# Optimization experiments

Hardware: AMD Instinct MI355X
Metric: run time of the kernel (lower is better)

## Reference

```python
import jax, jax.numpy as jnp
import numpy as np

jax.config.update("jax_enable_x64", True)  # I-BERT's FixedPointMul runs in double precision

# I-BERT IntSoftmax constants
COEF0 = 0.35815147
COEF1 = 0.96963238 / COEF0
COEF2 = 1.0 / COEF0
X0 = -0.6931          # -ln(2)
N_EXP = 30            # large integer n in int_exp
MAX_BIT = 32
OUTPUT_BIT = 8
ACT_BIT = 16

B, H, S = 1, 12, 2048


def sg(x):
    return jax.lax.stop_gradient(x)


def ste_round(x):
    # straight-through round (matches torch round_ste / SymmetricQuantFunction backward)
    return x + sg(jnp.round(x) - x)


def ste_floor(x):
    return x + sg(jnp.floor(x) - x)


def sym_scale(x_min, x_max, bits):
    # symmetric_linear_quantization_params: scale = clamp(max(|min|,|max|),1e-8)/(2^(b-1)-1)
    n = 2 ** (bits - 1) - 1
    s = jnp.maximum(jnp.abs(x_min), jnp.abs(x_max))
    return sg(jnp.maximum(s, 1e-8) / n)


def fixedpoint_mul(pre_act, pre_sf, z_sf, bits):
    # I-BERT fixedpoint_mul: requantize pre_act (granularity pre_sf) to scale z_sf
    # using a 31-bit mantissa frexp decomposition, computed in float64.
    n = 2 ** (bits - 1) - 1
    z_int = ste_round(pre_act.astype(jnp.float64) / pre_sf.astype(jnp.float64))
    new_scale = sg((pre_sf / z_sf).astype(jnp.float64))
    e = jnp.floor(jnp.log2(jnp.abs(new_scale))) + 1.0   # frexp exponent
    m_int = jnp.round((new_scale / 2.0 ** e) * 2.0 ** 31)  # 31-bit mantissa
    out = ste_round(z_int * m_int / 2.0 ** (31.0 - e))
    return jnp.clip(out, -n - 1, n).astype(jnp.float32)


def quant_softmax(x):
    n16 = 2 ** (ACT_BIT - 1) - 1
    # ---- outer QuantAct(16, symmetric), specified min/max = data min/max ----
    sf = sym_scale(sg(x.min()), sg(x.max()), ACT_BIT)
    x_int = jnp.clip(ste_round(x / sf), -n16 - 1, n16)
    quant_x = x_int * sf  # dequantized activation returned by QuantAct
    # ---- IntSoftmax ----
    xi = quant_x / sf
    xi = xi - xi.max(axis=-1, keepdims=True)
    # int_exp: shift-based exponential, exp(x) = 2^(-q) * exp(r), r in (-ln2, 0]
    x0_int = sg(jnp.floor(X0 / sf))               # negative integer
    xi = jnp.maximum(xi, N_EXP * x0_int)
    q = ste_floor(xi / x0_int)
    r = xi - x0_int * q
    # int_polynomial: 2nd-order poly approximation of exp on (-ln2, 0]
    b_int = sg(jnp.floor(COEF1 / sf))
    c_int = sg(jnp.floor(COEF2 / sf ** 2))
    z = r * (r + b_int) + c_int
    exp_sf = sg(COEF0 * sf ** 2) / 2.0 ** N_EXP
    exp_int = jnp.maximum(ste_floor(z * 2.0 ** (N_EXP - q)), 0.0)
    # ---- inner QuantAct(16): requantize exp to 16 bits to avoid overflow ----
    act_sf = sym_scale(sg(exp_int.min()), sg(exp_int.max()), ACT_BIT)
    exp_int16 = fixedpoint_mul(exp_int, exp_sf, act_sf, ACT_BIT)
    # ---- integer normalization to output_bit fixed point ----
    s = exp_int16.sum(axis=-1, keepdims=True)
    factor = ste_floor(2.0 ** MAX_BIT / s)
    out_int = ste_floor(exp_int16 * factor / 2.0 ** (MAX_BIT - OUTPUT_BIT))
    out_sf = 1.0 / 2.0 ** OUTPUT_BIT
    return out_int * out_sf  # softmax probs quantized to 1/256 grid


def setup_inputs() -> dict:
    key = jax.random.key(0)
    x = jax.random.normal(key, (B, H, S, S), dtype=jnp.float32)
    return {"x": x}


def reference(x):
    return quant_softmax(x)
```

## Files before the change

kernel.cpp:

```cpp
#include <hip/hip_runtime.h>
#include <math.h>


#define ROW_S 2048
#define MM_BLOCKS 2048
#define MM_STRIDE (MM_BLOCKS * 256)

typedef float floatx4 __attribute__((ext_vector_type(4)));

struct Scalars {
    double exp_sf_d;
    double inv_exp_sf;
    double m_int;
    double inv_pow;
    float  sf;
    float  inv_sf;
    float  x0_int;
    float  inv_x0;
    float  b_int;
    float  c_int;
    float  thirty_x0;
    float  _pad;
};

__device__ __forceinline__ float div_rn(float a, float b, float inv) {
    const float q0 = __fmul_rn(a, inv);
    const float r  = __fmaf_rn(-b, q0, a);
    return __fmaf_rn(r, inv, q0);
}
__device__ __forceinline__ double ddiv_rn(double a, double b, double inv) {
    const double q0 = __dmul_rn(a, inv);
    const double r  = __fma_rn(-b, q0, a);
    return __fma_rn(r, inv, q0);
}

__global__ __launch_bounds__(256) void k_amax(const float* __restrict__ x,
                                              float* __restrict__ pmax,
                                              int n4) {
    const int tid = threadIdx.x;
    const float4* x4 = (const float4*)x;
    float am = 0.0f;
    int i = blockIdx.x * 256 + tid;
    for (; i + 3 * MM_STRIDE < n4; i += 4 * MM_STRIDE) {
        const float4 v0 = x4[i];
        const float4 v1 = x4[i + MM_STRIDE];
        const float4 v2 = x4[i + 2 * MM_STRIDE];
        const float4 v3 = x4[i + 3 * MM_STRIDE];
        const float m0 = fmaxf(fmaxf(fabsf(v0.x), fabsf(v0.y)), fmaxf(fabsf(v0.z), fabsf(v0.w)));
        const float m1 = fmaxf(fmaxf(fabsf(v1.x), fabsf(v1.y)), fmaxf(fabsf(v1.z), fabsf(v1.w)));
        const float m2 = fmaxf(fmaxf(fabsf(v2.x), fabsf(v2.y)), fmaxf(fabsf(v2.z), fabsf(v2.w)));
        const float m3 = fmaxf(fmaxf(fabsf(v3.x), fabsf(v3.y)), fmaxf(fabsf(v3.z), fabsf(v3.w)));
        am = fmaxf(am, fmaxf(fmaxf(m0, m1), fmaxf(m2, m3)));
    }
    for (; i < n4; i += MM_STRIDE) {
        const float4 v = x4[i];
        am = fmaxf(am, fmaxf(fmaxf(fabsf(v.x), fabsf(v.y)), fmaxf(fabsf(v.z), fabsf(v.w))));
    }
#pragma unroll
    for (int m = 32; m > 0; m >>= 1) am = fmaxf(am, __shfl_xor(am, m));
    __shared__ float sred[4];
    const int wave = tid >> 6, lane = tid & 63;
    if (lane == 0) sred[wave] = am;
    __syncthreads();
    if (tid == 0)
        pmax[blockIdx.x] = fmaxf(fmaxf(sred[0], sred[1]), fmaxf(sred[2], sred[3]));
}

__global__ __launch_bounds__(256) void k_scalars(const float* __restrict__ pmax,
                                                 Scalars* __restrict__ sc) {
    const int tid = threadIdx.x;
    float am = 0.0f;
    for (int i = tid; i < MM_BLOCKS; i += 256) am = fmaxf(am, pmax[i]);
#pragma unroll
    for (int m = 32; m > 0; m >>= 1) am = fmaxf(am, __shfl_xor(am, m));
    __shared__ float sred[4];
    const int wave = tid >> 6, lane = tid & 63;
    if (lane == 0) sred[wave] = am;
    __syncthreads();
    if (tid == 0) {
        const float sabs = fmaxf(fmaxf(sred[0], sred[1]), fmaxf(sred[2], sred[3]));
        const float sf    = __fdiv_rn(fmaxf(sabs, 1e-8f), 32767.0f);
        const float x0i   = floorf(__fdiv_rn((float)(-0.6931), sf));
        const float sfsq  = __fmul_rn(sf, sf);
        const float b_int = floorf(__fdiv_rn((float)(0.96963238 / 0.35815147), sf));
        const float c_int = floorf(__fdiv_rn((float)(1.0 / 0.35815147), sfsq));
        const float exp_sf = __fdiv_rn(__fmul_rn((float)(0.35815147), sfsq), 1073741824.0f);
        const float emax   = __fmul_rn(c_int, 1073741824.0f);
        const float act_sf = __fdiv_rn(fmaxf(emax, 1e-8f), 32767.0f);
        const float  nsf = __fdiv_rn(exp_sf, act_sf);
        const double ns  = (double)nsf;
        int E;
        (void)frexp(ns, &E);
        const double m_int = rint(ldexp(ns, 31 - E));
        sc->exp_sf_d   = (double)exp_sf;
        sc->inv_exp_sf = 1.0 / (double)exp_sf;
        sc->m_int      = m_int;
        sc->inv_pow    = ldexp(1.0, E - 31);
        sc->sf         = sf;
        sc->inv_sf     = __fdiv_rn(1.0f, sf);
        sc->x0_int     = x0i;
        sc->inv_x0     = __fdiv_rn(1.0f, x0i);
        sc->b_int      = b_int;
        sc->c_int      = c_int;
        sc->thirty_x0  = __fmul_rn(30.0f, x0i);
    }
}

__global__ __launch_bounds__(256) void k_row(const float* __restrict__ x,
                                             float* __restrict__ out,
                                             const Scalars* __restrict__ scp) {
    const int lane = threadIdx.x & 63;
    const int wave = threadIdx.x >> 6;
    const size_t row = (size_t)blockIdx.x * 4 + wave;
    const floatx4* x4 = (const floatx4*)(x + row * ROW_S);
    floatx4* o4 = (floatx4*)(out + row * ROW_S);

    floatx4 v[8];
#pragma unroll
    for (int i = 0; i < 8; ++i) v[i] = x4[i * 64 + lane];

    const Scalars sc = *scp;
    const float sf = sc.sf, inv_sf = sc.inv_sf;

    float rmax = -INFINITY;
#pragma unroll
    for (int i = 0; i < 8; ++i) {
#pragma unroll
        for (int c = 0; c < 4; ++c) rmax = fmaxf(rmax, v[i][c]);
    }
#pragma unroll
    for (int m = 32; m > 0; m >>= 1) rmax = fmaxf(rmax, __shfl_xor(rmax, m));

    float t = rintf(div_rn(rmax, sf, inv_sf));
    t = fminf(fmaxf(t, -32768.0f), 32767.0f);
    t = __fmul_rn(t, sf);
    const float ximax = div_rn(t, sf, inv_sf);

    float ssum = 0.0f;
#pragma unroll
    for (int i = 0; i < 8; ++i) {
#pragma unroll
        for (int c = 0; c < 4; ++c) {
            float q = rintf(div_rn(v[i][c], sf, inv_sf));
            q = fminf(fmaxf(q, -32768.0f), 32767.0f);
            q = __fmul_rn(q, sf);
            const float xi = div_rn(q, sf, inv_sf);
            const float xs = __fsub_rn(xi, ximax);
            const float xm = fmaxf(xs, sc.thirty_x0);
            const float qf = floorf(div_rn(xm, sc.x0_int, sc.inv_x0));
            const float r  = __fsub_rn(xm, __fmul_rn(sc.x0_int, qf));
            const float z  = __fadd_rn(__fmul_rn(r, __fadd_rn(r, sc.b_int)), sc.c_int);
            const int   qi = (int)qf;
            const float p2 = __int_as_float((157 - qi) << 23);
            const float ei = fmaxf(floorf(__fmul_rn(z, p2)), 0.0f);
            const double a  = (double)ei;
            const double zi = rint(ddiv_rn(a, sc.exp_sf_d, sc.inv_exp_sf));
            double ovd = rint(__dmul_rn(__dmul_rn(zi, sc.m_int), sc.inv_pow));
            ovd = fmin(fmax(ovd, -32768.0), 32767.0);
            const float e16 = (float)ovd;
            v[i][c] = e16;
            ssum += e16;
        }
    }
#pragma unroll
    for (int m = 32; m > 0; m >>= 1) ssum += __shfl_xor(ssum, m);
    const float factor = floorf(__fdiv_rn(4294967296.0f, ssum));

#pragma unroll
    for (int i = 0; i < 8; ++i) {
        floatx4 w;
#pragma unroll
        for (int c = 0; c < 4; ++c) {
            const float oi = floorf(__fmul_rn(__fmul_rn(v[i][c], factor), 5.9604644775390625e-8f));
            w[c] = __fmul_rn(oi, 0.00390625f);
        }
        __builtin_nontemporal_store(w, &o4[i * 64 + lane]);
    }
}

extern "C" void kernel_launch(void* const* d_in, const int* in_sizes, int n_in,
                              void* d_out, int out_size, void* d_ws, size_t ws_size,
                              hipStream_t stream) {
    const float* x = (const float*)d_in[0];
    float* out = (float*)d_out;
    const int n = in_sizes[0];
    const int rows = n / ROW_S;

    Scalars* sc = (Scalars*)d_ws;
    float* pmax = (float*)((char*)d_ws + 256);

    k_amax<<<MM_BLOCKS, 256, 0, stream>>>(x, pmax, n / 4);
    k_scalars<<<1, 256, 0, stream>>>(pmax, sc);
    k_row<<<rows / 4, 256, 0, stream>>>(x, out, sc);
}
```

Before: 357.8 us.

## Fuse amax, scalar setup and row softmax into one cooperative persistent kernel

Replaces the three-kernel pipeline (global abs-max, scalar computation, per-row softmax) with a single cooperative kernel. It computes per-block maxima, does a grid-wide sync, has every block redundantly derive the quantization scalars, then loops persistently over row groups. This removes two kernel launches and the scalar round-trip through global memory. In exchange it adds a grid barrier and a persistent grid sized from occupancy, which may lower parallelism for the row phase. If the cooperative launch fails it falls back to the old three kernels.

```diff
diff --git a/kernel.cpp b/kernel.cpp
--- a/kernel.cpp
+++ b/kernel.cpp
@@ -1,10 +1,13 @@
 #include <hip/hip_runtime.h>
+#include <hip/hip_cooperative_groups.h>
 #include <math.h>
 
 
 #define ROW_S 2048
 #define MM_BLOCKS 2048
 #define MM_STRIDE (MM_BLOCKS * 256)
+
+namespace cg = cooperative_groups;
 
 typedef float floatx4 __attribute__((ext_vector_type(4)));
 
@@ -32,6 +35,144 @@
     const double q0 = __dmul_rn(a, inv);
     const double r  = __fma_rn(-b, q0, a);
     return __fma_rn(r, inv, q0);
+}
+
+__global__ __launch_bounds__(256) void k_fused(const float* __restrict__ x,
+                                               float* __restrict__ out,
+                                               float* __restrict__ pmax,
+                                               int n4, int ngroups) {
+    const int tid  = threadIdx.x;
+    const int lane = tid & 63, wave = tid >> 6;
+    const int G    = gridDim.x;
+    __shared__ float sred[4];
+
+    {
+        const float4* x4 = (const float4*)x;
+        const int stride = G * 256;
+        float am = 0.0f;
+        int i = blockIdx.x * 256 + tid;
+        for (; i + 3 * stride < n4; i += 4 * stride) {
+            const float4 v0 = x4[i];
+            const float4 v1 = x4[i + stride];
+            const float4 v2 = x4[i + 2 * stride];
+            const float4 v3 = x4[i + 3 * stride];
+            const float m0 = fmaxf(fmaxf(fabsf(v0.x), fabsf(v0.y)), fmaxf(fabsf(v0.z), fabsf(v0.w)));
+            const float m1 = fmaxf(fmaxf(fabsf(v1.x), fabsf(v1.y)), fmaxf(fabsf(v1.z), fabsf(v1.w)));
+            const float m2 = fmaxf(fmaxf(fabsf(v2.x), fabsf(v2.y)), fmaxf(fabsf(v2.z), fabsf(v2.w)));
+            const float m3 = fmaxf(fmaxf(fabsf(v3.x), fabsf(v3.y)), fmaxf(fabsf(v3.z), fabsf(v3.w)));
+            am = fmaxf(am, fmaxf(fmaxf(m0, m1), fmaxf(m2, m3)));
+        }
+        for (; i < n4; i += stride) {
+            const float4 v = x4[i];
+            am = fmaxf(am, fmaxf(fmaxf(fabsf(v.x), fabsf(v.y)), fmaxf(fabsf(v.z), fabsf(v.w))));
+        }
+#pragma unroll
+        for (int m = 32; m > 0; m >>= 1) am = fmaxf(am, __shfl_xor(am, m));
+        if (lane == 0) sred[wave] = am;
+        __syncthreads();
+        if (tid == 0) {
+            const float bm = fmaxf(fmaxf(sred[0], sred[1]), fmaxf(sred[2], sred[3]));
+            __hip_atomic_store(&pmax[blockIdx.x], bm,
+                               __ATOMIC_RELEASE, __HIP_MEMORY_SCOPE_AGENT);
+        }
+    }
+    cg::this_grid().sync();
+
+    float am = 0.0f;
+    for (int i = tid; i < G; i += 256)
+        am = fmaxf(am, __hip_atomic_load(&pmax[i],
+                       __ATOMIC_RELAXED, __HIP_MEMORY_SCOPE_AGENT));
+#pragma unroll
+    for (int m = 32; m > 0; m >>= 1) am = fmaxf(am, __shfl_xor(am, m));
+    if (lane == 0) sred[wave] = am;
+    __syncthreads();
+    const float sabs = fmaxf(fmaxf(sred[0], sred[1]), fmaxf(sred[2], sred[3]));
+
+    const float sf     = __fdiv_rn(fmaxf(sabs, 1e-8f), 32767.0f);
+    const float x0i    = floorf(__fdiv_rn((float)(-0.6931), sf));
+    const float sfsq   = __fmul_rn(sf, sf);
+    const float b_int  = floorf(__fdiv_rn((float)(0.96963238 / 0.35815147), sf));
+    const float c_int  = floorf(__fdiv_rn((float)(1.0 / 0.35815147), sfsq));
+    const float exp_sf = __fdiv_rn(__fmul_rn((float)(0.35815147), sfsq), 1073741824.0f);
+    const float emax   = __fmul_rn(c_int, 1073741824.0f);
+    const float act_sf = __fdiv_rn(fmaxf(emax, 1e-8f), 32767.0f);
+    const float  nsf = __fdiv_rn(exp_sf, act_sf);
+    const double ns  = (double)nsf;
+    int E;
+    (void)frexp(ns, &E);
+    const double m_int      = rint(ldexp(ns, 31 - E));
+    const double inv_pow    = ldexp(1.0, E - 31);
+    const double exp_sf_d   = (double)exp_sf;
+    const double inv_exp_sf = 1.0 / exp_sf_d;
+    const float  inv_sf     = __fdiv_rn(1.0f, sf);
+    const float  inv_x0     = __fdiv_rn(1.0f, x0i);
+    const float  thirty_x0  = __fmul_rn(30.0f, x0i);
+
+    for (int g = blockIdx.x; g < ngroups; g += G) {
+        const size_t row = (size_t)g * 4 + wave;
+        const floatx4* x4r = (const floatx4*)(x + row * ROW_S);
+        floatx4* o4 = (floatx4*)(out + row * ROW_S);
+
+        floatx4 v[8];
+#pragma unroll
+        for (int i = 0; i < 8; ++i) v[i] = x4r[i * 64 + lane];
+
+        float rmax = -INFINITY;
+#pragma unroll
+        for (int i = 0; i < 8; ++i) {
+#pragma unroll
+            for (int c = 0; c < 4; ++c) rmax = fmaxf(rmax, v[i][c]);
+        }
+#pragma unroll
+        for (int m = 32; m > 0; m >>= 1) rmax = fmaxf(rmax, __shfl_xor(rmax, m));
+
+        float t = rintf(div_rn(rmax, sf, inv_sf));
+        t = fminf(fmaxf(t, -32768.0f), 32767.0f);
+        t = __fmul_rn(t, sf);
+        const float ximax = div_rn(t, sf, inv_sf);
+
+        float ssum = 0.0f;
+#pragma unroll
+        for (int i = 0; i < 8; ++i) {
+#pragma unroll
+            for (int c = 0; c < 4; ++c) {
+                float q = rintf(div_rn(v[i][c], sf, inv_sf));
+                q = fminf(fmaxf(q, -32768.0f), 32767.0f);
+                q = __fmul_rn(q, sf);
+                const float xi = div_rn(q, sf, inv_sf);
+                const float xs = __fsub_rn(xi, ximax);
+                const float xm = fmaxf(xs, thirty_x0);
+                const float qf = floorf(div_rn(xm, x0i, inv_x0));
+                const float r  = __fsub_rn(xm, __fmul_rn(x0i, qf));
+                const float z  = __fadd_rn(__fmul_rn(r, __fadd_rn(r, b_int)), c_int);
+                const int   qi = (int)qf;
+                const float p2 = __int_as_float((157 - qi) << 23);
+                const float ei = fmaxf(floorf(__fmul_rn(z, p2)), 0.0f);
+                const double a  = (double)ei;
+                const double zi = rint(ddiv_rn(a, exp_sf_d, inv_exp_sf));
+                double ovd = rint(__dmul_rn(__dmul_rn(zi, m_int), inv_pow));
+                ovd = fmin(fmax(ovd, -32768.0), 32767.0);
+                const float e16 = (float)ovd;
+                v[i][c] = e16;
+                ssum += e16;
+            }
+        }
+#pragma unroll
+        for (int m = 32; m > 0; m >>= 1) ssum += __shfl_xor(ssum, m);
+        const float factor = floorf(__fdiv_rn(4294967296.0f, ssum));
+
+#pragma unroll
+        for (int i = 0; i < 8; ++i) {
+            floatx4 w;
+#pragma unroll
+            for (int c = 0; c < 4; ++c) {
+                const float oi = floorf(__fmul_rn(__fmul_rn(v[i][c], factor),
+                                                  5.9604644775390625e-8f));
+                w[c] = __fmul_rn(oi, 0.00390625f);
+            }
+            __builtin_nontemporal_store(w, &o4[i * 64 + lane]);
+        }
+    }
 }
 
 __global__ __launch_bounds__(256) void k_amax(const float* __restrict__ x,
@@ -185,11 +326,36 @@
     float* out = (float*)d_out;
     const int n = in_sizes[0];
     const int rows = n / ROW_S;
+    int n4 = n / 4;
+    int ngroups = rows / 4;
+
+    static int G = 0;
+    if (G == 0) {
+        int maxb = 0;
+        if (hipOccupancyMaxActiveBlocksPerMultiprocessor(
+                &maxb, reinterpret_cast<const void*>(k_fused), 256, 0) != hipSuccess ||
+            maxb <= 0)
+            maxb = 4;
+        int dev = 0, ncu = 0;
+        hipGetDevice(&dev);
+        if (hipDeviceGetAttribute(&ncu, hipDeviceAttributeMultiprocessorCount, dev) != hipSuccess ||
+            ncu <= 0)
+            ncu = 256;
+        const long cap = (long)maxb * ncu;
+        const int snaps[] = {2048, 1536, 1024, 768, 512, 384, 256};
+        G = 256;
+        for (int s : snaps) { if (cap >= s) { G = s; break; } }
+    }
+
+    float* pmaxc = (float*)d_ws;
+    void* args[] = {(void*)&x, (void*)&out, (void*)&pmaxc, (void*)&n4, (void*)&ngroups};
+    const hipError_t e = hipLaunchCooperativeKernel(
+        reinterpret_cast<const void*>(k_fused), dim3(G), dim3(256), args, 0, stream);
+    if (e == hipSuccess) return;
 
     Scalars* sc = (Scalars*)d_ws;
     float* pmax = (float*)((char*)d_ws + 256);
-
-    k_amax<<<MM_BLOCKS, 256, 0, stream>>>(x, pmax, n / 4);
+    k_amax<<<MM_BLOCKS, 256, 0, stream>>>(x, pmax, n4);
     k_scalars<<<1, 256, 0, stream>>>(pmax, sc);
     k_row<<<rows / 4, 256, 0, stream>>>(x, out, sc);
 }
```

Result: slower. 455.8 us (+27.4%).

## Fold scalar-derivation kernel into row kernel and deepen amax unrolling

Applied to the files above, without the earlier changes.

Removes the single-block k_scalars launch. Each row block now reduces the 2048 partial maxima itself and computes the quantization scalars redundantly, using readfirstlane to keep them in scalar registers. The amax pass also issues 8 loads in flight per iteration instead of 4. This saves a launch and a serialized tiny kernel, at the cost of every row block re-reading 8 KB of partials and repeating the scalar math, including double-precision divisions.

```diff
diff --git a/kernel.cpp b/kernel.cpp
--- a/kernel.cpp
+++ b/kernel.cpp
@@ -7,21 +7,6 @@
 #define MM_STRIDE (MM_BLOCKS * 256)
 
 typedef float floatx4 __attribute__((ext_vector_type(4)));
-
-struct Scalars {
-    double exp_sf_d;
-    double inv_exp_sf;
-    double m_int;
-    double inv_pow;
-    float  sf;
-    float  inv_sf;
-    float  x0_int;
-    float  inv_x0;
-    float  b_int;
-    float  c_int;
-    float  thirty_x0;
-    float  _pad;
-};
 
 __device__ __forceinline__ float div_rn(float a, float b, float inv) {
     const float q0 = __fmul_rn(a, inv);
@@ -34,6 +19,18 @@
     return __fma_rn(r, inv, q0);
 }
 
+__device__ __forceinline__ float rfl(float v) {
+    return __uint_as_float(__builtin_amdgcn_readfirstlane(__float_as_uint(v)));
+}
+__device__ __forceinline__ double rfld(double v) {
+    union { double d; unsigned long long u; } c;
+    c.d = v;
+    const unsigned lo = __builtin_amdgcn_readfirstlane((unsigned)c.u);
+    const unsigned hi = __builtin_amdgcn_readfirstlane((unsigned)(c.u >> 32));
+    c.u = ((unsigned long long)hi << 32) | lo;
+    return c.d;
+}
+
 __global__ __launch_bounds__(256) void k_amax(const float* __restrict__ x,
                                               float* __restrict__ pmax,
                                               int n4) {
@@ -41,20 +38,23 @@
     const float4* x4 = (const float4*)x;
     float am = 0.0f;
     int i = blockIdx.x * 256 + tid;
-    for (; i + 3 * MM_STRIDE < n4; i += 4 * MM_STRIDE) {
-        const float4 v0 = x4[i];
-        const float4 v1 = x4[i + MM_STRIDE];
-        const float4 v2 = x4[i + 2 * MM_STRIDE];
-        const float4 v3 = x4[i + 3 * MM_STRIDE];
-        const float m0 = fmaxf(fmaxf(fabsf(v0.x), fabsf(v0.y)), fmaxf(fabsf(v0.z), fabsf(v0.w)));
-        const float m1 = fmaxf(fmaxf(fabsf(v1.x), fabsf(v1.y)), fmaxf(fabsf(v1.z), fabsf(v1.w)));
-        const float m2 = fmaxf(fmaxf(fabsf(v2.x), fabsf(v2.y)), fmaxf(fabsf(v2.z), fabsf(v2.w)));
-        const float m3 = fmaxf(fmaxf(fabsf(v3.x), fabsf(v3.y)), fmaxf(fabsf(v3.z), fabsf(v3.w)));
-        am = fmaxf(am, fmaxf(fmaxf(m0, m1), fmaxf(m2, m3)));
+    for (; i + 7 * MM_STRIDE < n4; i += 8 * MM_STRIDE) {
+        float4 v[8];
+#pragma unroll
+        for (int u = 0; u < 8; ++u) v[u] = x4[i + u * MM_STRIDE];
+        float m[8];
+#pragma unroll
+        for (int u = 0; u < 8; ++u)
+            m[u] = fmaxf(fmaxf(fabsf(v[u].x), fabsf(v[u].y)),
+                         fmaxf(fabsf(v[u].z), fabsf(v[u].w)));
+        const float a0 = fmaxf(fmaxf(m[0], m[1]), fmaxf(m[2], m[3]));
+        const float a1 = fmaxf(fmaxf(m[4], m[5]), fmaxf(m[6], m[7]));
+        am = fmaxf(am, fmaxf(a0, a1));
     }
     for (; i < n4; i += MM_STRIDE) {
         const float4 v = x4[i];
-        am = fmaxf(am, fmaxf(fmaxf(fabsf(v.x), fabsf(v.y)), fmaxf(fabsf(v.z), fabsf(v.w))));
+        am = fmaxf(am, fmaxf(fmaxf(fabsf(v.x), fabsf(v.y)),
+                             fmaxf(fabsf(v.z), fabsf(v.w))));
     }
 #pragma unroll
     for (int m = 32; m > 0; m >>= 1) am = fmaxf(am, __shfl_xor(am, m));
@@ -66,61 +66,47 @@
         pmax[blockIdx.x] = fmaxf(fmaxf(sred[0], sred[1]), fmaxf(sred[2], sred[3]));
 }
 
-__global__ __launch_bounds__(256) void k_scalars(const float* __restrict__ pmax,
-                                                 Scalars* __restrict__ sc) {
-    const int tid = threadIdx.x;
+__global__ __launch_bounds__(256) void k_row(const float* __restrict__ x,
+                                             float* __restrict__ out,
+                                             const float* __restrict__ pmax) {
+    const int tid  = threadIdx.x;
+    const int lane = tid & 63, wave = tid >> 6;
+    const size_t row = (size_t)blockIdx.x * 4 + wave;
+    const floatx4* x4r = (const floatx4*)(x + row * ROW_S);
+    floatx4* o4 = (floatx4*)(out + row * ROW_S);
+
+    floatx4 v[8];
+#pragma unroll
+    for (int i = 0; i < 8; ++i) v[i] = x4r[i * 64 + lane];
+
+    __shared__ float sred[4];
     float am = 0.0f;
     for (int i = tid; i < MM_BLOCKS; i += 256) am = fmaxf(am, pmax[i]);
 #pragma unroll
     for (int m = 32; m > 0; m >>= 1) am = fmaxf(am, __shfl_xor(am, m));
-    __shared__ float sred[4];
-    const int wave = tid >> 6, lane = tid & 63;
     if (lane == 0) sred[wave] = am;
     __syncthreads();
-    if (tid == 0) {
-        const float sabs = fmaxf(fmaxf(sred[0], sred[1]), fmaxf(sred[2], sred[3]));
-        const float sf    = __fdiv_rn(fmaxf(sabs, 1e-8f), 32767.0f);
-        const float x0i   = floorf(__fdiv_rn((float)(-0.6931), sf));
-        const float sfsq  = __fmul_rn(sf, sf);
-        const float b_int = floorf(__fdiv_rn((float)(0.96963238 / 0.35815147), sf));
-        const float c_int = floorf(__fdiv_rn((float)(1.0 / 0.35815147), sfsq));
-        const float exp_sf = __fdiv_rn(__fmul_rn((float)(0.35815147), sfsq), 1073741824.0f);
-        const float emax   = __fmul_rn(c_int, 1073741824.0f);
-        const float act_sf = __fdiv_rn(fmaxf(emax, 1e-8f), 32767.0f);
-        const float  nsf = __fdiv_rn(exp_sf, act_sf);
-        const double ns  = (double)nsf;
-        int E;
-        (void)frexp(ns, &E);
-        const double m_int = rint(ldexp(ns, 31 - E));
-        sc->exp_sf_d   = (double)exp_sf;
-        sc->inv_exp_sf = 1.0 / (double)exp_sf;
-        sc->m_int      = m_int;
-        sc->inv_pow    = ldexp(1.0, E - 31);
-        sc->sf         = sf;
-        sc->inv_sf     = __fdiv_rn(1.0f, sf);
-        sc->x0_int     = x0i;
-        sc->inv_x0     = __fdiv_rn(1.0f, x0i);
-        sc->b_int      = b_int;
-        sc->c_int      = c_int;
-        sc->thirty_x0  = __fmul_rn(30.0f, x0i);
-    }
-}
+    const float sabs = fmaxf(fmaxf(sred[0], sred[1]), fmaxf(sred[2], sred[3]));
 
-__global__ __launch_bounds__(256) void k_row(const float* __restrict__ x,
-                                             float* __restrict__ out,
-                                             const Scalars* __restrict__ scp) {
-    const int lane = threadIdx.x & 63;
-    const int wave = threadIdx.x >> 6;
-    const size_t row = (size_t)blockIdx.x * 4 + wave;
-    const floatx4* x4 = (const floatx4*)(x + row * ROW_S);
-    floatx4* o4 = (floatx4*)(out + row * ROW_S);
-
-    floatx4 v[8];
-#pragma unroll
-    for (int i = 0; i < 8; ++i) v[i] = x4[i * 64 + lane];
-
-    const Scalars sc = *scp;
-    const float sf = sc.sf, inv_sf = sc.inv_sf;
+    const float sf     = rfl(__fdiv_rn(fmaxf(sabs, 1e-8f), 32767.0f));
+    const float x0i    = rfl(floorf(__fdiv_rn((float)(-0.6931), sf)));
+    const float sfsq   = __fmul_rn(sf, sf);
+    const float b_int  = rfl(floorf(__fdiv_rn((float)(0.96963238 / 0.35815147), sf)));
+    const float c_int  = rfl(floorf(__fdiv_rn((float)(1.0 / 0.35815147), sfsq)));
+    const float exp_sf = rfl(__fdiv_rn(__fmul_rn((float)(0.35815147), sfsq), 1073741824.0f));
+    const float emax   = __fmul_rn(c_int, 1073741824.0f);
+    const float act_sf = __fdiv_rn(fmaxf(emax, 1e-8f), 32767.0f);
+    const float  nsf = __fdiv_rn(exp_sf, act_sf);
+    const double ns  = (double)nsf;
+    int E;
+    (void)frexp(ns, &E);
+    const double m_int      = rfld(rint(ldexp(ns, 31 - E)));
+    const double inv_pow    = rfld(ldexp(1.0, E - 31));
+    const double exp_sf_d   = rfld((double)exp_sf);
+    const double inv_exp_sf = rfld(1.0 / (double)exp_sf);
+    const float  inv_sf     = rfl(__fdiv_rn(1.0f, sf));
+    const float  inv_x0     = rfl(__fdiv_rn(1.0f, x0i));
+    const float  thirty_x0  = rfl(__fmul_rn(30.0f, x0i));
 
     float rmax = -INFINITY;
 #pragma unroll
@@ -146,16 +132,16 @@
             q = __fmul_rn(q, sf);
             const float xi = div_rn(q, sf, inv_sf);
             const float xs = __fsub_rn(xi, ximax);
-            const float xm = fmaxf(xs, sc.thirty_x0);
-            const float qf = floorf(div_rn(xm, sc.x0_int, sc.inv_x0));
-            const float r  = __fsub_rn(xm, __fmul_rn(sc.x0_int, qf));
-            const float z  = __fadd_rn(__fmul_rn(r, __fadd_rn(r, sc.b_int)), sc.c_int);
+            const float xm = fmaxf(xs, thirty_x0);
+            const float qf = floorf(div_rn(xm, x0i, inv_x0));
+            const float r  = __fsub_rn(xm, __fmul_rn(x0i, qf));
+            const float z  = __fadd_rn(__fmul_rn(r, __fadd_rn(r, b_int)), c_int);
             const int   qi = (int)qf;
             const float p2 = __int_as_float((157 - qi) << 23);
             const float ei = fmaxf(floorf(__fmul_rn(z, p2)), 0.0f);
             const double a  = (double)ei;
-            const double zi = rint(ddiv_rn(a, sc.exp_sf_d, sc.inv_exp_sf));
-            double ovd = rint(__dmul_rn(__dmul_rn(zi, sc.m_int), sc.inv_pow));
+            const double zi = rint(ddiv_rn(a, exp_sf_d, inv_exp_sf));
+            double ovd = rint(__dmul_rn(__dmul_rn(zi, m_int), inv_pow));
             ovd = fmin(fmax(ovd, -32768.0), 32767.0);
             const float e16 = (float)ovd;
             v[i][c] = e16;
@@ -171,7 +157,8 @@
         floatx4 w;
 #pragma unroll
         for (int c = 0; c < 4; ++c) {
-            const float oi = floorf(__fmul_rn(__fmul_rn(v[i][c], factor), 5.9604644775390625e-8f));
+            const float oi = floorf(__fmul_rn(__fmul_rn(v[i][c], factor),
+                                              5.9604644775390625e-8f));
             w[c] = __fmul_rn(oi, 0.00390625f);
         }
         __builtin_nontemporal_store(w, &o4[i * 64 + lane]);
@@ -186,10 +173,8 @@
     const int n = in_sizes[0];
     const int rows = n / ROW_S;
 
-    Scalars* sc = (Scalars*)d_ws;
-    float* pmax = (float*)((char*)d_ws + 256);
+    float* pmax = (float*)d_ws;
 
     k_amax<<<MM_BLOCKS, 256, 0, stream>>>(x, pmax, n / 4);
-    k_scalars<<<1, 256, 0, stream>>>(pmax, sc);
-    k_row<<<rows / 4, 256, 0, stream>>>(x, out, sc);
+    k_row<<<rows / 4, 256, 0, stream>>>(x, out, pmax);
 }
```

After: 379.6 us. +6.1%, slower.
